# Kernel optimization log

Hardware: AMD Instinct MI355X
Metric: run time of the kernel (lower is better)

Reference implementation:

```python
import jax, jax.numpy as jnp
import numpy as np
import math

B, S, H = 4, 4096, 64
WINDOW = 2


def setup_inputs() -> dict:
    key = jax.random.key(0)
    ks = jax.random.split(key, 7)
    s = 0.05
    return {
        "feature": jax.random.normal(ks[0], (B, S, H), dtype=jnp.float32),
        "Wq": jax.random.normal(ks[1], (H, H), dtype=jnp.float32) * s,
        "bq": jax.random.normal(ks[2], (H,), dtype=jnp.float32) * s,
        "Wk": jax.random.normal(ks[3], (H, H), dtype=jnp.float32) * s,
        "bk": jax.random.normal(ks[4], (H,), dtype=jnp.float32) * s,
        "Wv": jax.random.normal(ks[5], (H, H), dtype=jnp.float32) * s,
        "bv": jax.random.normal(ks[6], (H,), dtype=jnp.float32) * s,
    }


def reference(feature, Wq, bq, Wk, bk, Wv, bv):
    b, seq, d_k = feature.shape
    # torch nn.Linear: y = x @ W.T + b
    q = feature @ Wq.T + bq  # [B,S,H]
    k = feature @ Wk.T + bk
    v = feature @ Wv.T + bv

    # banded 0/1 mask, |i-j| <= window, then softmax over the FULL row
    # (faithful to the original: zeros outside the band also get exp(0)=1 weight)
    idx = jnp.arange(seq)
    band = (jnp.abs(idx[:, None] - idx[None, :]) <= WINDOW).astype(jnp.float32)  # [S,S]
    weights = jax.nn.softmax(band, axis=-1)  # [S,S]

    # locally-averaged K: weights @ k, shared across batch
    mixed_k = jnp.einsum('st,bth->bsh', weights, k)  # [B,S,H]
    scores = jnp.einsum('bsh,bth->bst', q, mixed_k) / math.sqrt(d_k)  # [B,S,S]
    attn = jax.nn.softmax(scores, axis=-1)
    out = jnp.einsum('bst,bth->bsh', attn, v)  # [B,S,H]
    return out
```

## Files before the change

### kernel.cpp

```cpp
#include <hip/hip_runtime.h>
#include <hip/hip_bf16.h>
#include <math.h>

#define SEQ 4096
#define HD  64
#define NBATCH 4

#define EM1  1.71828182845904523536f
#define INVD5 (1.0f/(4096.f + 5.f*EM1))
#define INVD4 (1.0f/(4096.f + 4.f*EM1))
#define INVD3 (1.0f/(4096.f + 3.f*EM1))

typedef __attribute__((ext_vector_type(8))) short short8;
typedef __attribute__((ext_vector_type(4))) float f32x4;

__device__ __forceinline__ f32x4 mfma16(short8 a, short8 b, f32x4 c) {
    return __builtin_amdgcn_mfma_f32_16x16x32_bf16(a, b, c, 0, 0, 0);
}

__device__ __forceinline__ short bfs(float x) {
    __hip_bfloat16 h = __float2bfloat16(x);
    return *(short*)&h;
}

__device__ __forceinline__ short8 pack8(float4 a, float4 b) {
    short8 r;
    r[0] = bfs(a.x); r[1] = bfs(a.y); r[2] = bfs(a.z); r[3] = bfs(a.w);
    r[4] = bfs(b.x); r[5] = bfs(b.y); r[6] = bfs(b.z); r[7] = bfs(b.w);
    return r;
}

__device__ __forceinline__ float blo(unsigned v) { return __uint_as_float(v << 16); }
__device__ __forceinline__ float bhi(unsigned v) { return __uint_as_float(v & 0xffff0000u); }

__global__ __launch_bounds__(64) void proj_kernel(
    const float* __restrict__ feat,
    const float* __restrict__ Wq, const float* __restrict__ bq,
    const float* __restrict__ Wk, const float* __restrict__ bk,
    const float* __restrict__ Wv, const float* __restrict__ bv,
    __hip_bfloat16* __restrict__ qsb, __hip_bfloat16* __restrict__ ktb,
    __hip_bfloat16* __restrict__ vtb,
    float* __restrict__ kpart, float* __restrict__ vpart)
{
    __shared__ __hip_bfloat16 tscr[16 * 66];

    const int tid  = threadIdx.x;
    const int quad = tid >> 4, ln = tid & 15;
    const int mi = blockIdx.y;
    const int R0 = blockIdx.x * 16;
    const int b  = R0 >> 12;
    const int t0 = R0 & (SEQ - 1);

    const float* W    = (mi == 0) ? Wq : (mi == 1) ? Wk : Wv;
    const float* bias = (mi == 0) ? bq : (mi == 1) ? bk : bv;

    short8 af0, af1;
    {
        const float* fp = feat + (size_t)(R0 + ln) * HD + quad * 8;
        af0 = pack8(*(const float4*)(fp),      *(const float4*)(fp + 4));
        af1 = pack8(*(const float4*)(fp + 32), *(const float4*)(fp + 36));
    }

    float colsum[4];
    #pragma unroll
    for (int ct = 0; ct < 4; ++ct) {
        const int col = ct * 16 + ln;
        const float* wp = W + (size_t)col * HD + quad * 8;
        short8 b0 = pack8(*(const float4*)(wp),      *(const float4*)(wp + 4));
        short8 b1 = pack8(*(const float4*)(wp + 32), *(const float4*)(wp + 36));
        f32x4 c = {};
        c = mfma16(af0, b0, c);
        c = mfma16(af1, b1, c);
        const float bl = bias[col];

        if (mi == 0) {
            #pragma unroll
            for (int r = 0; r < 4; ++r)
                qsb[(size_t)(R0 + quad * 4 + r) * HD + col] =
                    __float2bfloat16((c[r] + bl) * 0.125f);
        } else {
            float tot = c[0] + c[1] + c[2] + c[3];
            tot += __shfl_xor(tot, 16);
            tot += __shfl_xor(tot, 32);
            colsum[ct] = tot;
            #pragma unroll
            for (int r = 0; r < 4; ++r)
                tscr[(quad * 4 + r) * 66 + col] = __float2bfloat16(c[r] + bl);
        }
    }

    if (mi != 0) {
        __syncthreads();
        float* part = (mi == 1) ? kpart : vpart;
        if (quad == 0) {
            #pragma unroll
            for (int ct = 0; ct < 4; ++ct) {
                const int col = ct * 16 + ln;
                part[(size_t)blockIdx.x * 64 + col] = colsum[ct] + 16.f * bias[col];
            }
        }
        __hip_bfloat16* dst = (mi == 1) ? ktb : vtb;
        #pragma unroll
        for (int i = 0; i < 2; ++i) {
            const int tsk = i * 64 + tid;
            const int hh = tsk >> 1, c8 = tsk & 1;
            short8 vv;
            #pragma unroll
            for (int j = 0; j < 8; ++j)
                vv[j] = *(const short*)&tscr[(c8 * 8 + j) * 66 + hh];
            *(short8*)(dst + ((size_t)(b * HD + hh)) * SEQ + t0 + c8 * 8) = vv;
        }
    }
}

__global__ __launch_bounds__(256) void mkernel(
    const __hip_bfloat16* __restrict__ ktb, const __hip_bfloat16* __restrict__ vtb,
    const float* __restrict__ kpart, float* __restrict__ Mpart)
{
    __shared__ float kts[64 * 38];
    __shared__ __hip_bfloat16 mkt[64 * 40];
    __shared__ __hip_bfloat16 vts[64 * 40];
    __shared__ float ktl[64];
    __shared__ float red[4][64];

    const int tid = threadIdx.x;
    const int b = blockIdx.y, chunk = blockIdx.x;
    const int t0 = chunk * 32;
    const int h = tid & 63, g = tid >> 6;

    {
        float kp = 0.f;
        for (int j = 0; j < 64; ++j)
            kp += kpart[(size_t)(b * 256 + g * 64 + j) * 64 + h];
        red[g][h] = kp;
    }

    for (int i = tid; i < 64 * 18; i += 256) {
        const int r = i / 18, c = i - r * 18;
        const int gt = t0 - 2 + c * 2;
        unsigned val = 0;
        if (gt >= 0 && gt <= SEQ - 2)
            val = *(const unsigned*)(ktb + (size_t)(b * 64 + r) * SEQ + gt);
        kts[r * 38 + c * 2]     = blo(val);
        kts[r * 38 + c * 2 + 1] = bhi(val);
    }
    {
        const int r = tid >> 2, c = tid & 3;
        *(uint4*)&vts[r * 40 + c * 8] =
            ((const uint4*)(vtb + (size_t)(b * 64 + r) * SEQ + t0))[c];
    }
    __syncthreads();
    if (tid < 64) ktl[tid] = red[0][tid] + red[1][tid] + red[2][tid] + red[3][tid];
    __syncthreads();

    {
        const int tb = g * 8;
        float w[12];
        #pragma unroll
        for (int j = 0; j < 12; ++j) w[j] = kts[h * 38 + tb + j];
        const float ktv = ktl[h];
        short8 o;
        #pragma unroll
        for (int i = 0; i < 8; ++i) {
            const int t = t0 + tb + i;
            float invD = INVD5;
            if (t < 2)            invD = (t == 0) ? INVD3 : INVD4;
            else if (t > SEQ - 3) invD = (t == SEQ - 1) ? INVD3 : INVD4;
            const float loc = w[i] + w[i+1] + w[i+2] + w[i+3] + w[i+4];
            o[i] = bfs((EM1 * loc + ktv) * invD);
        }
        *(short8*)&mkt[h * 40 + tb] = o;
    }
    __syncthreads();

    const int wave = g, lane = tid & 63, quad = lane >> 4, ln = lane & 15;
    short8 a = *(const short8*)&mkt[(wave * 16 + ln) * 40 + quad * 8];
    f32x4 acc[4] = {};
    #pragma unroll
    for (int ct = 0; ct < 4; ++ct) {
        short8 bb = *(const short8*)&vts[(ct * 16 + ln) * 40 + quad * 8];
        acc[ct] = mfma16(a, bb, acc[ct]);
    }
    const size_t mb = (size_t)(b * 128 + chunk) * 4096;
    #pragma unroll
    for (int ct = 0; ct < 4; ++ct)
        #pragma unroll
        for (int r = 0; r < 4; ++r)
            Mpart[mb + (size_t)(wave * 16 + quad * 4 + r) * 64 + ct * 16 + ln] = acc[ct][r];
}

__global__ __launch_bounds__(256) void mreduce_kernel(
    const float* __restrict__ Mpart, const float* __restrict__ kpart,
    const float* __restrict__ vpart, const __hip_bfloat16* __restrict__ ktb,
    __hip_bfloat16* __restrict__ MT, float* __restrict__ Vtot)
{
    __shared__ float red[4][64];
    const int b = blockIdx.y, h1 = blockIdx.x;
    const int tid = threadIdx.x;
    const int g = tid >> 6, h2 = tid & 63;

    float s = 0.f;
    for (int c = 0; c < 32; ++c)
        s += Mpart[(size_t)(b * 128 + g * 32 + c) * 4096 + h1 * 64 + h2];
    red[g][h2] = s;
    __syncthreads();
    if (tid < 64)
        MT[(size_t)b * 5120 + tid * 64 + h1] =
            __float2bfloat16(red[0][tid] + red[1][tid] + red[2][tid] + red[3][tid]);

    if (h1 == 0 && tid < 64) {
        const int hh = tid;
        float kt = 0.f;
        for (int j = 0; j < 256; ++j)
            kt += kpart[(size_t)(b * 256 + j) * 64 + hh];
        const __hip_bfloat16* kr = ktb + (size_t)(b * 64 + hh) * SEQ;
        const float e0 = __bfloat162float(kr[0]), e1 = __bfloat162float(kr[1]);
        const float e2 = __bfloat162float(kr[2]), e3 = __bfloat162float(kr[3]);
        const float f0 = __bfloat162float(kr[SEQ-4]), f1 = __bfloat162float(kr[SEQ-3]);
        const float f2 = __bfloat162float(kr[SEQ-2]), f3 = __bfloat162float(kr[SEQ-1]);
        const float Sint = 5.f*kt - 4.f*e0 - 3.f*e1 - 2.f*e2 - e3
                         - f0 - 2.f*f1 - 3.f*f2 - 4.f*f3;
        const float SlocD = Sint * INVD5
                          + (e0+e1+e2 + f1+f2+f3) * INVD3
                          + (e0+e1+e2+e3 + f0+f1+f2+f3) * INVD4;
        const float mktot = kt * (4092.f*INVD5 + 2.f*INVD4 + 2.f*INVD3) + EM1 * SlocD;
        MT[(size_t)b * 5120 + 64 * 64 + hh] = __float2bfloat16(mktot);
    }
    if (h1 == 1 && tid < 64) {
        float s2 = 0.f;
        for (int j = 0; j < 256; ++j)
            s2 += vpart[(size_t)(b * 256 + j) * 64 + tid];
        Vtot[b * 64 + tid] = s2;
    }
    if (h1 == 2) {
        for (int i = tid; i < 15 * 64; i += 256)
            MT[(size_t)b * 5120 + 65 * 64 + i] = __float2bfloat16(0.f);
    }
}

__global__ __launch_bounds__(64) void out_kernel(
    const __hip_bfloat16* __restrict__ qsb, const __hip_bfloat16* __restrict__ MT,
    const float* __restrict__ Vtot, float* __restrict__ out)
{
    const int tid = threadIdx.x;
    const int quad = tid >> 4, ln = tid & 15;
    const int R0 = blockIdx.x * 16;
    const int b = R0 >> 12;

    short8 qa0, qa1;
    {
        const __hip_bfloat16* qp = qsb + (size_t)(R0 + ln) * HD + quad * 8;
        qa0 = *(const short8*)qp;
        qa1 = *(const short8*)(qp + 32);
    }

    const __hip_bfloat16* mtb = MT + (size_t)b * 5120;
    f32x4 acc[5] = {};
    #pragma unroll
    for (int ct = 0; ct < 5; ++ct) {
        short8 b0 = *(const short8*)(mtb + (ct * 16 + ln) * 64 + quad * 8);
        short8 b1 = *(const short8*)(mtb + (ct * 16 + ln) * 64 + 32 + quad * 8);
        acc[ct] = mfma16(qa0, b0, acc[ct]);
        acc[ct] = mfma16(qa1, b1, acc[ct]);
    }

    float vt[4];
    #pragma unroll
    for (int ct = 0; ct < 4; ++ct) vt[ct] = Vtot[b * 64 + ct * 16 + ln];

    float inv[4];
    #pragma unroll
    for (int r = 0; r < 4; ++r) {
        const float den = __shfl(acc[4][r], tid & 48);
        inv[r] = 1.f / (4096.f + den);
    }
    #pragma unroll
    for (int ct = 0; ct < 4; ++ct)
        #pragma unroll
        for (int r = 0; r < 4; ++r)
            out[(size_t)(R0 + quad * 4 + r) * HD + ct * 16 + ln] =
                (vt[ct] + acc[ct][r]) * inv[r];
}

extern "C" void kernel_launch(void* const* d_in, const int* in_sizes, int n_in,
                              void* d_out, int out_size, void* d_ws, size_t ws_size,
                              hipStream_t stream)
{
    const float* feat = (const float*)d_in[0];
    const float* Wq = (const float*)d_in[1];
    const float* bq = (const float*)d_in[2];
    const float* Wk = (const float*)d_in[3];
    const float* bk = (const float*)d_in[4];
    const float* Wv = (const float*)d_in[5];
    const float* bv = (const float*)d_in[6];
    float* out = (float*)d_out;

    char* ws = (char*)d_ws;
    __hip_bfloat16* qsb   = (__hip_bfloat16*)(ws + 0);
    __hip_bfloat16* ktb   = (__hip_bfloat16*)(ws + (2u << 20));
    __hip_bfloat16* vtb   = (__hip_bfloat16*)(ws + (4u << 20));
    float*          kpart = (float*)(ws + (6u << 20));
    float*          vpart = (float*)(ws + (6u << 20) + 262144);
    float*          Mpart = (float*)(ws + (6u << 20) + 524288);
    __hip_bfloat16* MT    = (__hip_bfloat16*)(ws + (14u << 20) + 524288);
    float*          Vtot  = (float*)(ws + (14u << 20) + 524288 + 40960);

    proj_kernel<<<dim3(1024, 3), dim3(64), 0, stream>>>(
        feat, Wq, bq, Wk, bk, Wv, bv, qsb, ktb, vtb, kpart, vpart);
    mkernel<<<dim3(128, NBATCH), dim3(256), 0, stream>>>(ktb, vtb, kpart, Mpart);
    mreduce_kernel<<<dim3(64, NBATCH), dim3(256), 0, stream>>>(
        Mpart, kpart, vpart, ktb, MT, Vtot);
    out_kernel<<<dim3(1024), dim3(64), 0, stream>>>(qsb, MT, Vtot, out);
}
```

Before: 98.58 us.

## Fuse QKV projection per block and move band weighting onto V side

```diff
diff --git a/kernel.cpp b/kernel.cpp
--- a/kernel.cpp
+++ b/kernel.cpp
@@ -6,7 +6,7 @@
 #define HD  64
 #define NBATCH 4
 
-#define EM1  1.71828182845904523536f
+#define EM1   1.71828182845904523536f
 #define INVD5 (1.0f/(4096.f + 5.f*EM1))
 #define INVD4 (1.0f/(4096.f + 4.f*EM1))
 #define INVD3 (1.0f/(4096.f + 3.f*EM1))
@@ -32,8 +32,9 @@
 
 __device__ __forceinline__ float blo(unsigned v) { return __uint_as_float(v << 16); }
 __device__ __forceinline__ float bhi(unsigned v) { return __uint_as_float(v & 0xffff0000u); }
-
-__global__ __launch_bounds__(64) void proj_kernel(
+__device__ __forceinline__ float b2f(__hip_bfloat16 h) { return __bfloat162float(h); }
+
+__global__ __launch_bounds__(128) void proj_kernel(
     const float* __restrict__ feat,
     const float* __restrict__ Wq, const float* __restrict__ bq,
     const float* __restrict__ Wk, const float* __restrict__ bk,
@@ -42,157 +43,227 @@
     __hip_bfloat16* __restrict__ vtb,
     float* __restrict__ kpart, float* __restrict__ vpart)
 {
-    __shared__ __hip_bfloat16 tscr[16 * 66];
+    __shared__ __hip_bfloat16 tscr[32 * 66];
+    __shared__ float kred[2][64];
 
     const int tid  = threadIdx.x;
-    const int quad = tid >> 4, ln = tid & 15;
-    const int mi = blockIdx.y;
-    const int R0 = blockIdx.x * 16;
+    const int wave = tid >> 6, lane = tid & 63;
+    const int quad = lane >> 4, ln = lane & 15;
+    const int R0 = blockIdx.x * 32;
     const int b  = R0 >> 12;
     const int t0 = R0 & (SEQ - 1);
 
-    const float* W    = (mi == 0) ? Wq : (mi == 1) ? Wk : Wv;
-    const float* bias = (mi == 0) ? bq : (mi == 1) ? bk : bv;
-
     short8 af0, af1;
     {
-        const float* fp = feat + (size_t)(R0 + ln) * HD + quad * 8;
+        const float* fp = feat + (size_t)(R0 + wave * 16 + ln) * HD + quad * 8;
         af0 = pack8(*(const float4*)(fp),      *(const float4*)(fp + 4));
         af1 = pack8(*(const float4*)(fp + 32), *(const float4*)(fp + 36));
     }
 
-    float colsum[4];
-    #pragma unroll
-    for (int ct = 0; ct < 4; ++ct) {
-        const int col = ct * 16 + ln;
-        const float* wp = W + (size_t)col * HD + quad * 8;
-        short8 b0 = pack8(*(const float4*)(wp),      *(const float4*)(wp + 4));
-        short8 b1 = pack8(*(const float4*)(wp + 32), *(const float4*)(wp + 36));
-        f32x4 c = {};
-        c = mfma16(af0, b0, c);
-        c = mfma16(af1, b1, c);
-        const float bl = bias[col];
-
-        if (mi == 0) {
+    const float* Ws[3] = {Wq, Wk, Wv};
+    const float* Bs[3] = {bq, bk, bv};
+
+    #pragma unroll
+    for (int m = 0; m < 3; ++m) {
+        const float* W = Ws[m];
+        const float* bias = Bs[m];
+        #pragma unroll
+        for (int ct = 0; ct < 4; ++ct) {
+            const int col = ct * 16 + ln;
+            const float* wp = W + (size_t)col * HD + quad * 8;
+            short8 b0 = pack8(*(const float4*)(wp),      *(const float4*)(wp + 4));
+            short8 b1 = pack8(*(const float4*)(wp + 32), *(const float4*)(wp + 36));
+            f32x4 c = {};
+            c = mfma16(af0, b0, c);
+            c = mfma16(af1, b1, c);
+            const float bl = bias[col];
+
+            if (m == 0) {
+                #pragma unroll
+                for (int r = 0; r < 4; ++r)
+                    qsb[(size_t)(R0 + wave * 16 + quad * 4 + r) * HD + col] =
+                        __float2bfloat16((c[r] + bl) * 0.125f);
+            } else {
+                float tot = c[0] + c[1] + c[2] + c[3];
+                tot += __shfl_xor(tot, 16);
+                tot += __shfl_xor(tot, 32);
+                if (quad == 0) kred[wave][col] = tot;
+                #pragma unroll
+                for (int r = 0; r < 4; ++r)
+                    tscr[(wave * 16 + quad * 4 + r) * 66 + col] =
+                        __float2bfloat16(c[r] + bl);
+            }
+        }
+        if (m > 0) {
+            __syncthreads();
+            if (tid < 64)
+                ((m == 1) ? kpart : vpart)[(size_t)blockIdx.x * 64 + tid] =
+                    kred[0][tid] + kred[1][tid] + 32.f * bias[tid];
+            __hip_bfloat16* dst = (m == 1) ? ktb : vtb;
             #pragma unroll
-            for (int r = 0; r < 4; ++r)
-                qsb[(size_t)(R0 + quad * 4 + r) * HD + col] =
-                    __float2bfloat16((c[r] + bl) * 0.125f);
-        } else {
-            float tot = c[0] + c[1] + c[2] + c[3];
-            tot += __shfl_xor(tot, 16);
-            tot += __shfl_xor(tot, 32);
-            colsum[ct] = tot;
-            #pragma unroll
-            for (int r = 0; r < 4; ++r)
-                tscr[(quad * 4 + r) * 66 + col] = __float2bfloat16(c[r] + bl);
-        }
-    }
-
-    if (mi != 0) {
-        __syncthreads();
-        float* part = (mi == 1) ? kpart : vpart;
-        if (quad == 0) {
-            #pragma unroll
-            for (int ct = 0; ct < 4; ++ct) {
-                const int col = ct * 16 + ln;
-                part[(size_t)blockIdx.x * 64 + col] = colsum[ct] + 16.f * bias[col];
-            }
-        }
-        __hip_bfloat16* dst = (mi == 1) ? ktb : vtb;
-        #pragma unroll
-        for (int i = 0; i < 2; ++i) {
-            const int tsk = i * 64 + tid;
-            const int hh = tsk >> 1, c8 = tsk & 1;
-            short8 vv;
-            #pragma unroll
-            for (int j = 0; j < 8; ++j)
-                vv[j] = *(const short*)&tscr[(c8 * 8 + j) * 66 + hh];
-            *(short8*)(dst + ((size_t)(b * HD + hh)) * SEQ + t0 + c8 * 8) = vv;
+            for (int i = 0; i < 2; ++i) {
+                const int tsk = i * 128 + tid;
+                const int hh = tsk >> 2, c8 = tsk & 3;
+                short8 vv;
+                #pragma unroll
+                for (int j = 0; j < 8; ++j)
+                    vv[j] = *(const short*)&tscr[(c8 * 8 + j) * 66 + hh];
+                *(short8*)(dst + ((size_t)(b * HD + hh)) * SEQ + t0 + c8 * 8) = vv;
+            }
+            __syncthreads();
         }
     }
 }
 
 __global__ __launch_bounds__(256) void mkernel(
     const __hip_bfloat16* __restrict__ ktb, const __hip_bfloat16* __restrict__ vtb,
-    const float* __restrict__ kpart, float* __restrict__ Mpart)
-{
-    __shared__ float kts[64 * 38];
-    __shared__ __hip_bfloat16 mkt[64 * 40];
-    __shared__ __hip_bfloat16 vts[64 * 40];
-    __shared__ float ktl[64];
-    __shared__ float red[4][64];
+    const float* __restrict__ kpart, const float* __restrict__ vpart,
+    __hip_bfloat16* __restrict__ Mpart, float* __restrict__ Mcorr,
+    __hip_bfloat16* __restrict__ MT, float* __restrict__ Vtot)
+{
+    __shared__ float vws[64 * 38];
+    __shared__ __hip_bfloat16 lvt[64 * 40];
+    __shared__ float scr[4][64];
+    __shared__ float ktl[64], vtl[64];
+    __shared__ float lc[4][64], vv_e[4][64];
 
     const int tid = threadIdx.x;
+
+    if (blockIdx.y == 4) {
+        if (blockIdx.x >= 16) return;
+        const int b = blockIdx.x >> 2, slab = blockIdx.x & 3;
+        const int h = tid & 63, g = tid >> 6;
+
+        if (slab == 0 || slab == 3) {
+            float kp = 0.f;
+            for (int j = 0; j < 32; ++j)
+                kp += kpart[(size_t)(b * 128 + g * 32 + j) * 64 + h];
+            scr[g][h] = kp;
+            __syncthreads();
+            if (tid < 64) ktl[tid] = scr[0][tid] + scr[1][tid] + scr[2][tid] + scr[3][tid];
+        }
+        if (slab == 0) {
+            __syncthreads();
+            if (tid < 64) {
+                const int hh = tid;
+                const float kt = ktl[hh];
+                const __hip_bfloat16* kr = ktb + (size_t)(b * 64 + hh) * SEQ;
+                const float e0 = b2f(kr[0]), e1 = b2f(kr[1]), e2 = b2f(kr[2]), e3 = b2f(kr[3]);
+                const float f0 = b2f(kr[SEQ-4]), f1 = b2f(kr[SEQ-3]);
+                const float f2 = b2f(kr[SEQ-2]), f3 = b2f(kr[SEQ-1]);
+                const float Sint = 5.f*kt - 4.f*e0 - 3.f*e1 - 2.f*e2 - e3
+                                 - f0 - 2.f*f1 - 3.f*f2 - 4.f*f3;
+                const float SlocD = Sint * INVD5
+                                  + (e0+e1+e2 + f1+f2+f3) * INVD3
+                                  + (e0+e1+e2+e3 + f0+f1+f2+f3) * INVD4;
+                const float mktot = kt * (4092.f*INVD5 + 2.f*INVD4 + 2.f*INVD3) + EM1 * SlocD;
+                MT[(size_t)b * 5120 + 64 * 64 + hh] = __float2bfloat16(mktot);
+            }
+        } else if (slab == 1) {
+            float vp = 0.f;
+            for (int j = 0; j < 32; ++j)
+                vp += vpart[(size_t)(b * 128 + g * 32 + j) * 64 + h];
+            scr[g][h] = vp;
+            __syncthreads();
+            if (tid < 64)
+                Vtot[b * 64 + tid] = scr[0][tid] + scr[1][tid] + scr[2][tid] + scr[3][tid];
+        } else if (slab == 2) {
+            for (int i = tid; i < 15 * 64; i += 256)
+                MT[(size_t)b * 5120 + 65 * 64 + i] = __float2bfloat16(0.f);
+        } else {
+            __syncthreads();
+            {
+                float vp = 0.f;
+                for (int j = 0; j < 32; ++j)
+                    vp += vpart[(size_t)(b * 128 + g * 32 + j) * 64 + h];
+                scr[g][h] = vp;
+            }
+            __syncthreads();
+            if (tid < 64) vtl[tid] = scr[0][tid] + scr[1][tid] + scr[2][tid] + scr[3][tid];
+            if (tid < 64) {
+                const int hh = tid;
+                const __hip_bfloat16* kr = ktb + (size_t)(b * 64 + hh) * SEQ;
+                const float e0 = b2f(kr[0]), e1 = b2f(kr[1]), e2 = b2f(kr[2]), e3 = b2f(kr[3]);
+                const float f0 = b2f(kr[SEQ-4]), f1 = b2f(kr[SEQ-3]);
+                const float f2 = b2f(kr[SEQ-2]), f3 = b2f(kr[SEQ-1]);
+                lc[0][hh] = e0 + e1 + e2;
+                lc[1][hh] = e0 + e1 + e2 + e3;
+                lc[2][hh] = f0 + f1 + f2 + f3;
+                lc[3][hh] = f1 + f2 + f3;
+                const __hip_bfloat16* vr = vtb + (size_t)(b * 64 + hh) * SEQ;
+                vv_e[0][hh] = b2f(vr[0]);
+                vv_e[1][hh] = b2f(vr[1]);
+                vv_e[2][hh] = b2f(vr[SEQ-2]);
+                vv_e[3][hh] = b2f(vr[SEQ-1]);
+            }
+            __syncthreads();
+            const float dd3 = INVD3 - INVD5, dd4 = INVD4 - INVD5;
+            const int h1 = tid >> 2;
+            const float l0 = lc[0][h1], l1 = lc[1][h1], l2 = lc[2][h1], l3 = lc[3][h1];
+            const float kt1 = ktl[h1];
+            #pragma unroll
+            for (int j = 0; j < 16; ++j) {
+                const int h2 = (tid & 3) * 16 + j;
+                const float VD = INVD5 * vtl[h2]
+                               + dd3 * (vv_e[0][h2] + vv_e[3][h2])
+                               + dd4 * (vv_e[1][h2] + vv_e[2][h2]);
+                const float mc = EM1 * (dd3 * (l0 * vv_e[0][h2] + l3 * vv_e[3][h2])
+                                      + dd4 * (l1 * vv_e[1][h2] + l2 * vv_e[2][h2]))
+                               + kt1 * VD;
+                Mcorr[(size_t)(b * 64 + h1) * 64 + h2] = mc;
+            }
+        }
+        return;
+    }
+
     const int b = blockIdx.y, chunk = blockIdx.x;
     const int t0 = chunk * 32;
-    const int h = tid & 63, g = tid >> 6;
-
-    {
-        float kp = 0.f;
-        for (int j = 0; j < 64; ++j)
-            kp += kpart[(size_t)(b * 256 + g * 64 + j) * 64 + h];
-        red[g][h] = kp;
-    }
 
     for (int i = tid; i < 64 * 18; i += 256) {
         const int r = i / 18, c = i - r * 18;
         const int gt = t0 - 2 + c * 2;
         unsigned val = 0;
         if (gt >= 0 && gt <= SEQ - 2)
-            val = *(const unsigned*)(ktb + (size_t)(b * 64 + r) * SEQ + gt);
-        kts[r * 38 + c * 2]     = blo(val);
-        kts[r * 38 + c * 2 + 1] = bhi(val);
-    }
+            val = *(const unsigned*)(vtb + (size_t)(b * 64 + r) * SEQ + gt);
+        vws[r * 38 + c * 2]     = blo(val);
+        vws[r * 38 + c * 2 + 1] = bhi(val);
+    }
+    __syncthreads();
+
     {
-        const int r = tid >> 2, c = tid & 3;
-        *(uint4*)&vts[r * 40 + c * 8] =
-            ((const uint4*)(vtb + (size_t)(b * 64 + r) * SEQ + t0))[c];
+        const int h = tid & 63, g = tid >> 6;
+        float w[12];
+        #pragma unroll
+        for (int j = 0; j < 12; ++j) w[j] = vws[h * 38 + g * 8 + j];
+        short8 o;
+        #pragma unroll
+        for (int i = 0; i < 8; ++i)
+            o[i] = bfs(w[i] + w[i+1] + w[i+2] + w[i+3] + w[i+4]);
+        *(short8*)&lvt[h * 40 + g * 8] = o;
     }
     __syncthreads();
-    if (tid < 64) ktl[tid] = red[0][tid] + red[1][tid] + red[2][tid] + red[3][tid];
-    __syncthreads();
-
-    {
-        const int tb = g * 8;
-        float w[12];
-        #pragma unroll
-        for (int j = 0; j < 12; ++j) w[j] = kts[h * 38 + tb + j];
-        const float ktv = ktl[h];
-        short8 o;
-        #pragma unroll
-        for (int i = 0; i < 8; ++i) {
-            const int t = t0 + tb + i;
-            float invD = INVD5;
-            if (t < 2)            invD = (t == 0) ? INVD3 : INVD4;
-            else if (t > SEQ - 3) invD = (t == SEQ - 1) ? INVD3 : INVD4;
-            const float loc = w[i] + w[i+1] + w[i+2] + w[i+3] + w[i+4];
-            o[i] = bfs((EM1 * loc + ktv) * invD);
-        }
-        *(short8*)&mkt[h * 40 + tb] = o;
-    }
-    __syncthreads();
-
-    const int wave = g, lane = tid & 63, quad = lane >> 4, ln = lane & 15;
-    short8 a = *(const short8*)&mkt[(wave * 16 + ln) * 40 + quad * 8];
+
+    const int wave = tid >> 6, lane = tid & 63, quad = lane >> 4, ln = lane & 15;
+    short8 a = *(const short8*)(ktb + (size_t)(b * 64 + wave * 16 + ln) * SEQ
+                                + t0 + quad * 8);
     f32x4 acc[4] = {};
     #pragma unroll
     for (int ct = 0; ct < 4; ++ct) {
-        short8 bb = *(const short8*)&vts[(ct * 16 + ln) * 40 + quad * 8];
+        short8 bb = *(const short8*)&lvt[(ct * 16 + ln) * 40 + quad * 8];
         acc[ct] = mfma16(a, bb, acc[ct]);
     }
-    const size_t mb = (size_t)(b * 128 + chunk) * 4096;
+    __hip_bfloat16* mp = Mpart + (size_t)(b * 128 + chunk) * 4096;
     #pragma unroll
     for (int ct = 0; ct < 4; ++ct)
         #pragma unroll
         for (int r = 0; r < 4; ++r)
-            Mpart[mb + (size_t)(wave * 16 + quad * 4 + r) * 64 + ct * 16 + ln] = acc[ct][r];
+            mp[(wave * 16 + quad * 4 + r) * 64 + ct * 16 + ln] =
+                __float2bfloat16(acc[ct][r]);
 }
 
 __global__ __launch_bounds__(256) void mreduce_kernel(
-    const float* __restrict__ Mpart, const float* __restrict__ kpart,
-    const float* __restrict__ vpart, const __hip_bfloat16* __restrict__ ktb,
-    __hip_bfloat16* __restrict__ MT, float* __restrict__ Vtot)
+    const __hip_bfloat16* __restrict__ Mpart, const float* __restrict__ Mcorr,
+    __hip_bfloat16* __restrict__ MT)
 {
     __shared__ float red[4][64];
     const int b = blockIdx.y, h1 = blockIdx.x;
@@ -200,41 +271,14 @@
     const int g = tid >> 6, h2 = tid & 63;
 
     float s = 0.f;
-    for (int c = 0; c < 32; ++c)
-        s += Mpart[(size_t)(b * 128 + g * 32 + c) * 4096 + h1 * 64 + h2];
+    for (int c = g * 32; c < g * 32 + 32; ++c)
+        s += b2f(Mpart[(size_t)(b * 128 + c) * 4096 + h1 * 64 + h2]);
     red[g][h2] = s;
     __syncthreads();
-    if (tid < 64)
-        MT[(size_t)b * 5120 + tid * 64 + h1] =
-            __float2bfloat16(red[0][tid] + red[1][tid] + red[2][tid] + red[3][tid]);
-
-    if (h1 == 0 && tid < 64) {
-        const int hh = tid;
-        float kt = 0.f;
-        for (int j = 0; j < 256; ++j)
-            kt += kpart[(size_t)(b * 256 + j) * 64 + hh];
-        const __hip_bfloat16* kr = ktb + (size_t)(b * 64 + hh) * SEQ;
-        const float e0 = __bfloat162float(kr[0]), e1 = __bfloat162float(kr[1]);
-        const float e2 = __bfloat162float(kr[2]), e3 = __bfloat162float(kr[3]);
-        const float f0 = __bfloat162float(kr[SEQ-4]), f1 = __bfloat162float(kr[SEQ-3]);
-        const float f2 = __bfloat162float(kr[SEQ-2]), f3 = __bfloat162float(kr[SEQ-1]);
-        const float Sint = 5.f*kt - 4.f*e0 - 3.f*e1 - 2.f*e2 - e3
-                         - f0 - 2.f*f1 - 3.f*f2 - 4.f*f3;
-        const float SlocD = Sint * INVD5
-                          + (e0+e1+e2 + f1+f2+f3) * INVD3
-                          + (e0+e1+e2+e3 + f0+f1+f2+f3) * INVD4;
-        const float mktot = kt * (4092.f*INVD5 + 2.f*INVD4 + 2.f*INVD3) + EM1 * SlocD;
-        MT[(size_t)b * 5120 + 64 * 64 + hh] = __float2bfloat16(mktot);
-    }
-    if (h1 == 1 && tid < 64) {
-        float s2 = 0.f;
-        for (int j = 0; j < 256; ++j)
-            s2 += vpart[(size_t)(b * 256 + j) * 64 + tid];
-        Vtot[b * 64 + tid] = s2;
-    }
-    if (h1 == 2) {
-        for (int i = tid; i < 15 * 64; i += 256)
-            MT[(size_t)b * 5120 + 65 * 64 + i] = __float2bfloat16(0.f);
+    if (tid < 64) {
+        const float m = (EM1 * INVD5) * (red[0][tid] + red[1][tid] + red[2][tid] + red[3][tid])
+                      + Mcorr[(size_t)(b * 64 + h1) * 64 + tid];
+        MT[(size_t)b * 5120 + tid * 64 + h1] = __float2bfloat16(m);
     }
 }
 
@@ -301,14 +345,15 @@
     __hip_bfloat16* vtb   = (__hip_bfloat16*)(ws + (4u << 20));
     float*          kpart = (float*)(ws + (6u << 20));
     float*          vpart = (float*)(ws + (6u << 20) + 262144);
-    float*          Mpart = (float*)(ws + (6u << 20) + 524288);
-    __hip_bfloat16* MT    = (__hip_bfloat16*)(ws + (14u << 20) + 524288);
-    float*          Vtot  = (float*)(ws + (14u << 20) + 524288 + 40960);
-
-    proj_kernel<<<dim3(1024, 3), dim3(64), 0, stream>>>(
+    __hip_bfloat16* Mpart = (__hip_bfloat16*)(ws + (6u << 20) + 524288);
+    float*          Mcorr = (float*)(ws + (10u << 20) + 524288);
+    __hip_bfloat16* MT    = (__hip_bfloat16*)(ws + (10u << 20) + 589824);
+    float*          Vtot  = (float*)(ws + (10u << 20) + 630784);
+
+    proj_kernel<<<dim3(512), dim3(128), 0, stream>>>(
         feat, Wq, bq, Wk, bk, Wv, bv, qsb, ktb, vtb, kpart, vpart);
-    mkernel<<<dim3(128, NBATCH), dim3(256), 0, stream>>>(ktb, vtb, kpart, Mpart);
-    mreduce_kernel<<<dim3(64, NBATCH), dim3(256), 0, stream>>>(
-        Mpart, kpart, vpart, ktb, MT, Vtot);
+    mkernel<<<dim3(128, 5), dim3(256), 0, stream>>>(
+        ktb, vtb, kpart, vpart, Mpart, Mcorr, MT, Vtot);
+    mreduce_kernel<<<dim3(64, NBATCH), dim3(256), 0, stream>>>(Mpart, Mcorr, MT);
     out_kernel<<<dim3(1024), dim3(64), 0, stream>>>(qsb, MT, Vtot, out);
 }
```

Result: faster. 89.61 us (-9.1%).
